# Performance work log

Measured on AMD Instinct MI355X. Metric: run time of the kernel, lower is better.

Reference implementation:

```python
import jax, jax.numpy as jnp
import numpy as np

DIM = 1024
NUM_HEADS = 16
HEAD_DIM = DIM // NUM_HEADS
B, T = 2, 2048


def _rope_tables(seq_len, head_dim, dtype=jnp.float32):
    inv_freq = 1.0 / (10000.0 ** (jnp.arange(0, head_dim, 2, dtype=jnp.float32) / head_dim))
    t = jnp.arange(seq_len, dtype=jnp.float32)
    freqs = jnp.einsum('i,j->ij', t, inv_freq)            # [T, head_dim/2]
    emb = jnp.concatenate((freqs, freqs), axis=-1)         # [T, head_dim]
    return jnp.cos(emb).astype(dtype), jnp.sin(emb).astype(dtype)


def _rotate_half(x):
    x1, x2 = x[..., : x.shape[-1] // 2], x[..., x.shape[-1] // 2 :]
    return jnp.concatenate((-x2, x1), axis=-1)


def setup_inputs() -> dict:
    key = jax.random.key(0)
    ks = jax.random.split(key, 5)
    s = 1.0 / np.sqrt(DIM)
    return {
        'x': jax.random.normal(ks[0], (B, T, DIM), dtype=jnp.float32),
        'w_q': jax.random.normal(ks[1], (DIM, DIM), dtype=jnp.float32) * s,
        'w_k': jax.random.normal(ks[2], (DIM, DIM), dtype=jnp.float32) * s,
        'w_v': jax.random.normal(ks[3], (DIM, DIM), dtype=jnp.float32) * s,
        'w_out': jax.random.normal(ks[4], (DIM, DIM), dtype=jnp.float32) * s,
    }


def reference(x, w_q, w_k, w_v, w_out):
    Bn, Tn, C = x.shape
    scale = HEAD_DIM ** -0.5
    # nn.Linear(bias=False): y = x @ W^T; reshape to [B, H, T, Dh]
    def proj(w):
        y = jnp.einsum('btc,dc->btd', x, w)
        return y.reshape(Bn, Tn, NUM_HEADS, HEAD_DIM).transpose(0, 2, 1, 3)
    q, k, v = proj(w_q), proj(w_k), proj(w_v)
    cos, sin = _rope_tables(Tn, HEAD_DIM, x.dtype)         # [T, Dh], broadcasts over B,H
    q = q * cos + _rotate_half(q) * sin
    k = k * cos + _rotate_half(k) * sin
    attn = jnp.einsum('bhqd,bhkd->bhqk', q, k) * scale     # [B,H,T,T]
    attn = jax.nn.softmax(attn, axis=-1)
    out = jnp.einsum('bhqk,bhkd->bhqd', attn, v)           # [B,H,T,Dh]
    out = out.transpose(0, 2, 1, 3).reshape(Bn, Tn, C)
    return jnp.einsum('btc,dc->btd', out, w_out)
```

## Files before the change

kernel.cpp:

```cpp
#include <hip/hip_runtime.h>


typedef _Float16 f16;
typedef f16 f16x8 __attribute__((ext_vector_type(8)));
typedef __fp16 fp16x2 __attribute__((ext_vector_type(2)));
typedef float f32x4 __attribute__((ext_vector_type(4)));
typedef float f32x16 __attribute__((ext_vector_type(16)));
typedef unsigned int u32;
typedef unsigned short u16;

union V16 { uint4 u; f16x8 h; };

__device__ __forceinline__ float exp2_fast(float x) {
#if __has_builtin(__builtin_amdgcn_exp2f)
  return __builtin_amdgcn_exp2f(x);
#else
  return __expf(x * 0.69314718056f);
#endif
}

__device__ __forceinline__ u32 pkrtz(float a, float b) {
  union { fp16x2 h; u32 u; } cv;
  cv.h = __builtin_amdgcn_cvt_pkrtz(a, b);
  return cv.u;
}

#define PLSWAP(a, b)                                                          \
  asm volatile("s_nop 1\n\tv_permlane32_swap_b32 %0, %1" : "+v"(a), "+v"(b))

#define GLDS(src, dst) __builtin_amdgcn_global_load_lds(                      \
    (const __attribute__((address_space(1))) void*)(const void*)(src),        \
    (__attribute__((address_space(3))) void*)(void*)(dst), 16, 0, 0)

__global__ __launch_bounds__(256) void rope_tables_kernel(float* __restrict__ cosT,
                                                          float* __restrict__ sinT) {
  int i = blockIdx.x * 256 + threadIdx.x;
  int t = i >> 5, j = i & 31;
  float inv = 1.0f / powf(10000.0f, (float)(2 * j) * (1.0f / 64.0f));
  float ang = (float)t * inv;
  double a = (double)ang;
  cosT[i] = (float)cos(a);
  sinT[i] = (float)sin(a);
}

__global__ __launch_bounds__(256)
void cvt5_kernel(const float* __restrict__ x,  const float* __restrict__ wq,
                 const float* __restrict__ wk, const float* __restrict__ wv,
                 const float* __restrict__ wo,
                 f16* __restrict__ xh, f16* __restrict__ W3,
                 f16* __restrict__ woh) {
  int bx = blockIdx.x;
  const float* src; f16* dst; int i;
  if (bx < 4096) {
    src = x; dst = xh; i = bx * 256 + threadIdx.x;
  } else {
    int b = (bx - 4096) >> 10;
    i = ((bx - 4096) & 1023) * 256 + threadIdx.x;
    src = (b == 0) ? wq : (b == 1) ? wk : (b == 2) ? wv : wo;
    dst = (b == 3) ? woh : W3 + (size_t)b * 1048576;
  }
  float4 v = ((const float4*)src)[i];
  union { f16 h[4]; uint2 u; } cv;
  cv.h[0] = (f16)v.x; cv.h[1] = (f16)v.y; cv.h[2] = (f16)v.z; cv.h[3] = (f16)v.w;
  ((uint2*)dst)[i] = cv.u;
}

__global__ __launch_bounds__(256)
void gemm_qkv_kernel(const f16* __restrict__ X,
                     const f16* __restrict__ W3,
                     f16* __restrict__ Qo, f16* __restrict__ Ko,
                     f16* __restrict__ VTo,
                     const float* __restrict__ cosT,
                     const float* __restrict__ sinT) {
  __shared__ u16 lds[2][8192];

  const int tid = threadIdx.x, lane = tid & 63, w = tid >> 6;
  const int c = lane & 15, g = lane >> 4;
  const int m0 = blockIdx.x * 128;
  const int by = blockIdx.y;
  const int wsel = by >> 3, hp = by & 7, h0 = hp * 2;
  const f16* Wb = W3 + (size_t)wsel * (1024 * 1024) + (size_t)hp * 128 * 1024;

  const int n1 = tid, n2 = tid + 256;
  const int r1 = n1 >> 2, gc1 = (n1 & 3) ^ ((n1 >> 3) & 3);
  const int r2 = n2 >> 2, gc2 = (n2 & 3) ^ ((n2 >> 3) & 3);
  const f16* gA1 = X + (size_t)(m0 + r1) * 1024 + gc1 * 8;
  const f16* gA2 = X + (size_t)(m0 + r2) * 1024 + gc2 * 8;
  const f16* gB1 = Wb + (size_t)r1 * 1024 + gc1 * 8;
  const f16* gB2 = Wb + (size_t)r2 * 1024 + gc2 * 8;
  const int dA1 = n1 * 8, dA2 = n2 * 8;
  const int dB1 = 4096 + n1 * 8, dB2 = 4096 + n2 * 8;

  f32x4 acc[2][8];
  const f32x4 zero = {0.f, 0.f, 0.f, 0.f};
#pragma unroll
  for (int mi = 0; mi < 2; ++mi)
#pragma unroll
    for (int ni = 0; ni < 8; ++ni) acc[mi][ni] = zero;

#define STAGE_QKV(buf, kt) do {                                               \
    const int ko = (kt) * 32;                                                 \
    GLDS(gA1 + ko, &lds[buf][dA1]);                                           \
    GLDS(gA2 + ko, &lds[buf][dA2]);                                           \
    GLDS(gB1 + ko, &lds[buf][dB1]);                                           \
    GLDS(gB2 + ko, &lds[buf][dB2]);                                           \
  } while (0)

  const int swz = (g ^ ((c >> 1) & 3)) * 8;

  STAGE_QKV(0, 0);
  __syncthreads();
  for (int kt = 0; kt < 32; ++kt) {
    const int cur = kt & 1;
    if (kt < 31) STAGE_QKV(cur ^ 1, kt + 1);
    V16 a[2], b[8];
#pragma unroll
    for (int mi = 0; mi < 2; ++mi)
      a[mi].u = *(const uint4*)&lds[cur][(w * 32 + mi * 16 + c) * 32 + swz];
#pragma unroll
    for (int ni = 0; ni < 8; ++ni)
      b[ni].u = *(const uint4*)&lds[cur][4096 + (ni * 16 + c) * 32 + swz];
    __builtin_amdgcn_s_setprio(1);
#pragma unroll
    for (int mi = 0; mi < 2; ++mi)
#pragma unroll
      for (int ni = 0; ni < 8; ++ni)
        acc[mi][ni] = __builtin_amdgcn_mfma_f32_16x16x32_f16(a[mi].h, b[ni].h, acc[mi][ni], 0, 0, 0);
    __builtin_amdgcn_s_setprio(0);
    __syncthreads();
  }

  if (wsel < 2) {
    f16* Out = (wsel == 0) ? Qo : Ko;
    const float psc = (wsel == 0) ? 0.18033688f : 1.0f;
#pragma unroll
    for (int mi = 0; mi < 2; ++mi)
#pragma unroll
      for (int r = 0; r < 4; ++r) {
        int m = m0 + w * 32 + mi * 16 + g * 4 + r;
        int bb = m >> 11, t = m & 2047;
        float co0 = cosT[t * 32 + c],      si0 = sinT[t * 32 + c];
        float co1 = cosT[t * 32 + 16 + c], si1 = sinT[t * 32 + 16 + c];
#pragma unroll
        for (int ni = 0; ni < 8; ++ni) {
          int head = h0 + (ni >> 2);
          int d = (ni & 3) * 16 + c;
          float co = (ni & 1) ? co1 : co0;
          float si = (ni & 1) ? si1 : si0;
          float partner = acc[mi][ni ^ 2][r];
          float v = (acc[mi][ni][r] * co + ((d < 32) ? -partner : partner) * si) * psc;
          Out[((size_t)(bb * 16 + head) * 2048 + t) * 64 + d] = (f16)v;
        }
      }
  } else {
    u16* sT = &lds[0][0];
    const int bbv = m0 >> 11;
    const int t0 = (m0 & 2047) + w * 32;
#pragma unroll
    for (int p = 0; p < 2; ++p) {
#pragma unroll
      for (int mi = 0; mi < 2; ++mi)
#pragma unroll
        for (int nn = 0; nn < 4; ++nn)
#pragma unroll
          for (int r = 0; r < 4; ++r) {
            int ni = p * 4 + nn;
            int dl = nn * 16 + c;
            int tl = mi * 16 + g * 4 + r;
            union { f16 h; u16 u; } cv; cv.h = (f16)acc[mi][ni][r];
            sT[w * 2560 + dl * 40 + tl] = cv.u;
          }
      f16* dst = VTo + ((size_t)(bbv * 16 + h0 + p) * 64 + lane) * 2048 + t0;
      const u16* srcp = &sT[w * 2560 + lane * 40];
      *(uint4*)(dst +  0) = *(const uint4*)(srcp +  0);
      *(uint4*)(dst +  8) = *(const uint4*)(srcp +  8);
      *(uint4*)(dst + 16) = *(const uint4*)(srcp + 16);
      *(uint4*)(dst + 24) = *(const uint4*)(srcp + 24);
    }
  }
}

__global__ __launch_bounds__(256)
void gemm_out_kernel(const f16* __restrict__ AH, const f16* __restrict__ BH,
                     float* __restrict__ outF) {
  __shared__ u16 lds[2][6144];

  const int tid = threadIdx.x, lane = tid & 63, w = tid >> 6;
  const int c = lane & 15, g = lane >> 4;
  const int m0 = blockIdx.x * 128, n0 = blockIdx.y * 64;

  const int n1 = tid, n2 = tid + 256;
  const int r1 = n1 >> 2, gc1 = (n1 & 3) ^ ((n1 >> 3) & 3);
  const int r2 = n2 >> 2, gc2 = (n2 & 3) ^ ((n2 >> 3) & 3);
  const f16* gA1 = AH + (size_t)(m0 + r1) * 1024 + gc1 * 8;
  const f16* gA2 = AH + (size_t)(m0 + r2) * 1024 + gc2 * 8;
  const f16* gB1 = BH + (size_t)(n0 + r1) * 1024 + gc1 * 8;
  const int dA1 = n1 * 8, dA2 = n2 * 8;
  const int dB1 = 4096 + n1 * 8;

  f32x4 acc[2][4];
  const f32x4 zero = {0.f, 0.f, 0.f, 0.f};
#pragma unroll
  for (int mi = 0; mi < 2; ++mi)
#pragma unroll
    for (int ni = 0; ni < 4; ++ni) acc[mi][ni] = zero;

#define STAGE_OUT(buf, kt) do {                                               \
    const int ko = (kt) * 32;                                                 \
    GLDS(gA1 + ko, &lds[buf][dA1]);                                           \
    GLDS(gA2 + ko, &lds[buf][dA2]);                                           \
    GLDS(gB1 + ko, &lds[buf][dB1]);                                           \
  } while (0)

  const int swz = (g ^ ((c >> 1) & 3)) * 8;

  STAGE_OUT(0, 0);
  __syncthreads();
  for (int kt = 0; kt < 32; ++kt) {
    const int cur = kt & 1;
    if (kt < 31) STAGE_OUT(cur ^ 1, kt + 1);
    V16 a[2], b[4];
#pragma unroll
    for (int mi = 0; mi < 2; ++mi)
      a[mi].u = *(const uint4*)&lds[cur][(w * 32 + mi * 16 + c) * 32 + swz];
#pragma unroll
    for (int ni = 0; ni < 4; ++ni)
      b[ni].u = *(const uint4*)&lds[cur][4096 + (ni * 16 + c) * 32 + swz];
    __builtin_amdgcn_s_setprio(1);
#pragma unroll
    for (int mi = 0; mi < 2; ++mi)
#pragma unroll
      for (int ni = 0; ni < 4; ++ni)
        acc[mi][ni] = __builtin_amdgcn_mfma_f32_16x16x32_f16(a[mi].h, b[ni].h, acc[mi][ni], 0, 0, 0);
    __builtin_amdgcn_s_setprio(0);
    __syncthreads();
  }

#pragma unroll
  for (int mi = 0; mi < 2; ++mi)
#pragma unroll
    for (int r = 0; r < 4; ++r) {
      int m = m0 + w * 32 + mi * 16 + g * 4 + r;
#pragma unroll
      for (int ni = 0; ni < 4; ++ni)
        outF[(size_t)m * 1024 + n0 + ni * 16 + c] = acc[mi][ni][r];
    }
}

__global__ __launch_bounds__(256)
void attn_kernel(const f16* __restrict__ Q, const f16* __restrict__ K,
                 const f16* __restrict__ VT, f16* __restrict__ OH) {
  __shared__ u16 sK[64 * 64];
  __shared__ u16 sV[64 * 64];
  __shared__ u16 sT16[4][32][36];

  const int tid = threadIdx.x, lane = tid & 63, wid = tid >> 6;
  const int q32 = lane & 31, hi = lane >> 5;
  const int hh = blockIdx.y, bb = blockIdx.z, bh = bb * 16 + hh;
  const int q0 = blockIdx.x * 128 + wid * 32;

  V16 qf[4];
  const f16* qp = Q + ((size_t)bh * 2048 + q0 + q32) * 64 + 8 * hi;
#pragma unroll
  for (int kd = 0; kd < 4; ++kd)
    qf[kd].u = *(const uint4*)(qp + 16 * kd);

  f32x16 o0 = 0.0f, o1 = 0.0f;
  float m_run = -1e30f, l_run = 0.f;

  const int srow = tid >> 3, scol = tid & 7;
  const f16* gK = K  + ((size_t)bh * 2048 + srow) * 64 + scol * 8;
  const f16* gV = VT + ((size_t)bh * 64 + srow) * 2048 + scol * 8;
  const int dst0 = srow * 128 + ((scol ^ (srow & 7)) << 4);
  const int dst1 = dst0 + 32 * 128;

  uint4 rk0, rk1, rv0, rv1;
#define LOADT(kt) do {                                                        \
    const f16* pk = gK + (size_t)(kt) * 4096;                                 \
    rk0 = *(const uint4*)(pk);                                                \
    rk1 = *(const uint4*)(pk + 32 * 64);                                      \
    const f16* pv = gV + (size_t)(kt) * 64;                                   \
    rv0 = *(const uint4*)(pv);                                                \
    rv1 = *(const uint4*)(pv + 32 * 2048);                                    \
  } while (0)
#define WRITET() do {                                                         \
    *(uint4*)((char*)sK + dst0) = rk0; *(uint4*)((char*)sK + dst1) = rk1;     \
    *(uint4*)((char*)sV + dst0) = rv0; *(uint4*)((char*)sV + dst1) = rv1;     \
  } while (0)

  const int swzrow = (q32 & 7) << 4;

  LOADT(0);
  WRITET();
  __syncthreads();

  for (int kt = 0; kt < 32; ++kt) {
    if (kt < 31) LOADT(kt + 1);

    f32x16 st0 = 0.0f, st1 = 0.0f;
    __builtin_amdgcn_s_setprio(1);
#pragma unroll
    for (int kd = 0; kd < 4; ++kd) {
      const int off = ((32 * kd + 16 * hi) ^ swzrow);
      V16 kf0, kf1;
      kf0.u = *(const uint4*)((const char*)sK + q32 * 128 + off);
      kf1.u = *(const uint4*)((const char*)sK + (32 + q32) * 128 + off);
      st0 = __builtin_amdgcn_mfma_f32_32x32x16_f16(kf0.h, qf[kd].h, st0, 0, 0, 0);
      st1 = __builtin_amdgcn_mfma_f32_32x32x16_f16(kf1.h, qf[kd].h, st1, 0, 0, 0);
    }
    __builtin_amdgcn_s_setprio(0);

    float mx = st0[0];
#pragma unroll
    for (int r = 1; r < 16; ++r) mx = fmaxf(mx, st0[r]);
#pragma unroll
    for (int r = 0; r < 16; ++r) mx = fmaxf(mx, st1[r]);
    mx = fmaxf(mx, __shfl_xor(mx, 32, 64));
    if (!__all(mx <= m_run + 11.5415603f)) {
      float mnew = fmaxf(m_run, mx);
      float alpha = exp2_fast(m_run - mnew);
      m_run = mnew;
      l_run *= alpha;
      o0 *= alpha;
      o1 *= alpha;
    }
    float sum = 0.f;
    u32 c0[8], c1[8];
#pragma unroll
    for (int m = 0; m < 8; ++m) {
      float p0 = exp2_fast(st0[2 * m] - m_run);
      float p1 = exp2_fast(st0[2 * m + 1] - m_run);
      sum += p0 + p1;
      c0[m] = pkrtz(p0, p1);
      float p2 = exp2_fast(st1[2 * m] - m_run);
      float p3 = exp2_fast(st1[2 * m + 1] - m_run);
      sum += p2 + p3;
      c1[m] = pkrtz(p2, p3);
    }
    sum += __shfl_xor(sum, 32, 64);
    l_run += sum;

    V16 pB[4];
    {
      u32 y0 = c0[0], x0 = c0[2]; PLSWAP(y0, x0);
      u32 y1 = c0[1], x1 = c0[3]; PLSWAP(y1, x1);
      pB[0].u.x = y0; pB[0].u.y = y1; pB[0].u.z = x0; pB[0].u.w = x1;
      u32 y2 = c0[4], x2 = c0[6]; PLSWAP(y2, x2);
      u32 y3 = c0[5], x3 = c0[7]; PLSWAP(y3, x3);
      pB[1].u.x = y2; pB[1].u.y = y3; pB[1].u.z = x2; pB[1].u.w = x3;
      u32 y4 = c1[0], x4 = c1[2]; PLSWAP(y4, x4);
      u32 y5 = c1[1], x5 = c1[3]; PLSWAP(y5, x5);
      pB[2].u.x = y4; pB[2].u.y = y5; pB[2].u.z = x4; pB[2].u.w = x5;
      u32 y6 = c1[4], x6 = c1[6]; PLSWAP(y6, x6);
      u32 y7 = c1[5], x7 = c1[7]; PLSWAP(y7, x7);
      pB[3].u.x = y6; pB[3].u.y = y7; pB[3].u.z = x6; pB[3].u.w = x7;
    }

    __builtin_amdgcn_s_setprio(1);
#pragma unroll
    for (int ks = 0; ks < 4; ++ks) {
      const int off = ((32 * ks + 16 * hi) ^ swzrow);
      V16 vf0, vf1;
      vf0.u = *(const uint4*)((const char*)sV + q32 * 128 + off);
      vf1.u = *(const uint4*)((const char*)sV + (32 + q32) * 128 + off);
      o0 = __builtin_amdgcn_mfma_f32_32x32x16_f16(vf0.h, pB[ks].h, o0, 0, 0, 0);
      o1 = __builtin_amdgcn_mfma_f32_32x32x16_f16(vf1.h, pB[ks].h, o1, 0, 0, 0);
    }
    __builtin_amdgcn_s_setprio(0);

    __syncthreads();
    if (kt < 31) WRITET();
    __syncthreads();
  }

  const float inv = 1.0f / l_run;
  const int qr = lane >> 1, dh = (lane & 1) * 16;
#pragma unroll
  for (int dt = 0; dt < 2; ++dt) {
#pragma unroll
    for (int r = 0; r < 16; ++r) {
      float v = (dt ? o1[r] : o0[r]) * inv;
      union { f16 h; u16 u; } cv; cv.h = (f16)v;
      sT16[wid][q32][(r & 3) + 8 * (r >> 2) + 4 * hi] = cv.u;
    }
    __syncthreads();
    const u16* sp = &sT16[wid][qr][dh];
    uint2 a0 = *(const uint2*)(sp + 0),  a1 = *(const uint2*)(sp + 4);
    uint2 a2 = *(const uint2*)(sp + 8),  a3 = *(const uint2*)(sp + 12);
    size_t gbase = ((size_t)bb * 2048 + q0 + qr) * 1024 + hh * 64 + 32 * dt + dh;
    *(uint2*)(OH + gbase + 0)  = a0;
    *(uint2*)(OH + gbase + 4)  = a1;
    *(uint2*)(OH + gbase + 8)  = a2;
    *(uint2*)(OH + gbase + 12) = a3;
    __syncthreads();
  }
}

extern "C" void kernel_launch(void* const* d_in, const int* in_sizes, int n_in,
                              void* d_out, int out_size, void* d_ws, size_t ws_size,
                              hipStream_t stream) {
  const float* x  = (const float*)d_in[0];
  const float* wq = (const float*)d_in[1];
  const float* wk = (const float*)d_in[2];
  const float* wv = (const float*)d_in[3];
  const float* wo = (const float*)d_in[4];

  constexpr size_t SZ_X   = 4096ull * 1024 * 2;
  constexpr size_t SZ_W   = 1024ull * 1024 * 2;
  constexpr size_t SZ_QKV = 2ull * 16 * 2048 * 64 * 2;
  constexpr size_t SZ_TBL = 2048ull * 32 * 4;
  constexpr size_t NEED = SZ_X + 4 * SZ_W + 3 * SZ_QKV + 2 * SZ_TBL;
  if (ws_size < NEED) return;

  char* ws = (char*)d_ws;
  f16* xh  = (f16*)(ws);
  f16* W3  = (f16*)(ws + SZ_X);
  f16* woh = (f16*)(ws + SZ_X + 3 * SZ_W);
  char* p  = ws + SZ_X + 4 * SZ_W;
  f16* qb  = (f16*)(p);            p += SZ_QKV;
  f16* kb  = (f16*)(p);            p += SZ_QKV;
  f16* vT  = (f16*)(p);            p += SZ_QKV;
  float* cosT = (float*)(p);       p += SZ_TBL;
  float* sinT = (float*)(p);
  f16* oh = xh;

  rope_tables_kernel<<<256, 256, 0, stream>>>(cosT, sinT);
  cvt5_kernel<<<8192, 256, 0, stream>>>(x, wq, wk, wv, wo, xh, W3, woh);

  gemm_qkv_kernel<<<dim3(32, 24), 256, 0, stream>>>(xh, W3, qb, kb, vT,
                                                    cosT, sinT);

  attn_kernel<<<dim3(16, 16, 2), 256, 0, stream>>>(qb, kb, vT, oh);

  gemm_out_kernel<<<dim3(32, 16), 256, 0, stream>>>(oh, woh, (float*)d_out);
}
```

Baseline: 137.8 us.

## Software-pipeline attention with triple-buffered K/V and overlapped QK^T/PV

```diff
diff --git a/kernel.cpp b/kernel.cpp
--- a/kernel.cpp
+++ b/kernel.cpp
@@ -247,17 +247,19 @@
     }
 }
 
-__global__ __launch_bounds__(256)
+__global__ __launch_bounds__(256, 2)
 void attn_kernel(const f16* __restrict__ Q, const f16* __restrict__ K,
                  const f16* __restrict__ VT, f16* __restrict__ OH) {
-  __shared__ u16 sK[64 * 64];
-  __shared__ u16 sV[64 * 64];
+  __shared__ u16 sKV[3][8192];
   __shared__ u16 sT16[4][32][36];
 
   const int tid = threadIdx.x, lane = tid & 63, wid = tid >> 6;
   const int q32 = lane & 31, hi = lane >> 5;
-  const int hh = blockIdx.y, bb = blockIdx.z, bh = bb * 16 + hh;
-  const int q0 = blockIdx.x * 128 + wid * 32;
+  const int bx = blockIdx.x;
+  const int bh = (bx & 7) + 8 * (bx >> 7);
+  const int qt = (bx >> 3) & 15;
+  const int bb = bh >> 4, hh = bh & 15;
+  const int q0 = qt * 128 + wid * 32;
 
   V16 qf[4];
   const f16* qp = Q + ((size_t)bh * 2048 + q0 + q32) * 64 + 8 * hi;
@@ -283,95 +285,105 @@
     rv0 = *(const uint4*)(pv);                                                \
     rv1 = *(const uint4*)(pv + 32 * 2048);                                    \
   } while (0)
-#define WRITET() do {                                                         \
-    *(uint4*)((char*)sK + dst0) = rk0; *(uint4*)((char*)sK + dst1) = rk1;     \
-    *(uint4*)((char*)sV + dst0) = rv0; *(uint4*)((char*)sV + dst1) = rv1;     \
+#define WRITET(buf) do {                                                      \
+    char* base_ = (char*)&sKV[buf][0];                                        \
+    *(uint4*)(base_ + dst0) = rk0; *(uint4*)(base_ + dst1) = rk1;             \
+    *(uint4*)(base_ + 8192 + dst0) = rv0; *(uint4*)(base_ + 8192 + dst1) = rv1;\
   } while (0)
 
   const int swzrow = (q32 & 7) << 4;
 
+#define QKT(D0, D1, buf) do {                                                 \
+    const char* kb_ = (const char*)&sKV[buf][0];                              \
+    __builtin_amdgcn_s_setprio(1);                                            \
+    _Pragma("unroll")                                                         \
+    for (int kd = 0; kd < 4; ++kd) {                                          \
+      const int off = ((32 * kd + 16 * hi) ^ swzrow);                         \
+      V16 kf0, kf1;                                                           \
+      kf0.u = *(const uint4*)(kb_ + q32 * 128 + off);                         \
+      kf1.u = *(const uint4*)(kb_ + (32 + q32) * 128 + off);                  \
+      D0 = __builtin_amdgcn_mfma_f32_32x32x16_f16(kf0.h, qf[kd].h, D0, 0, 0, 0);\
+      D1 = __builtin_amdgcn_mfma_f32_32x32x16_f16(kf1.h, qf[kd].h, D1, 0, 0, 0);\
+    }                                                                         \
+    __builtin_amdgcn_s_setprio(0);                                            \
+  } while (0)
+
+#define SOFTMAX_PB() do {                                                     \
+    float mx = st0[0];                                                        \
+    _Pragma("unroll")                                                         \
+    for (int r = 1; r < 16; ++r) mx = fmaxf(mx, st0[r]);                      \
+    _Pragma("unroll")                                                         \
+    for (int r = 0; r < 16; ++r) mx = fmaxf(mx, st1[r]);                      \
+    mx = fmaxf(mx, __shfl_xor(mx, 32, 64));                                   \
+    if (!__all(mx <= m_run + 11.5415603f)) {                                  \
+      float mnew = fmaxf(m_run, mx);                                          \
+      float alpha = exp2_fast(m_run - mnew);                                  \
+      m_run = mnew; l_run *= alpha; o0 *= alpha; o1 *= alpha;                 \
+    }                                                                         \
+    float sum = 0.f;                                                          \
+    u32 c0[8], c1[8];                                                         \
+    _Pragma("unroll")                                                         \
+    for (int m = 0; m < 8; ++m) {                                             \
+      float p0 = exp2_fast(st0[2 * m] - m_run);                               \
+      float p1 = exp2_fast(st0[2 * m + 1] - m_run);                           \
+      sum += p0 + p1; c0[m] = pkrtz(p0, p1);                                  \
+      float p2 = exp2_fast(st1[2 * m] - m_run);                               \
+      float p3 = exp2_fast(st1[2 * m + 1] - m_run);                           \
+      sum += p2 + p3; c1[m] = pkrtz(p2, p3);                                  \
+    }                                                                         \
+    sum += __shfl_xor(sum, 32, 64);                                           \
+    l_run += sum;                                                             \
+    { u32 y0 = c0[0], x0 = c0[2]; PLSWAP(y0, x0);                             \
+      u32 y1 = c0[1], x1 = c0[3]; PLSWAP(y1, x1);                             \
+      pB[0].u.x = y0; pB[0].u.y = y1; pB[0].u.z = x0; pB[0].u.w = x1;         \
+      u32 y2 = c0[4], x2 = c0[6]; PLSWAP(y2, x2);                             \
+      u32 y3 = c0[5], x3 = c0[7]; PLSWAP(y3, x3);                             \
+      pB[1].u.x = y2; pB[1].u.y = y3; pB[1].u.z = x2; pB[1].u.w = x3;         \
+      u32 y4 = c1[0], x4 = c1[2]; PLSWAP(y4, x4);                             \
+      u32 y5 = c1[1], x5 = c1[3]; PLSWAP(y5, x5);                             \
+      pB[2].u.x = y4; pB[2].u.y = y5; pB[2].u.z = x4; pB[2].u.w = x5;         \
+      u32 y6 = c1[4], x6 = c1[6]; PLSWAP(y6, x6);                             \
+      u32 y7 = c1[5], x7 = c1[7]; PLSWAP(y7, x7);                             \
+      pB[3].u.x = y6; pB[3].u.y = y7; pB[3].u.z = x6; pB[3].u.w = x7; }       \
+  } while (0)
+
+#define PVOP(buf) do {                                                        \
+    const char* vb_ = (const char*)&sKV[buf][0] + 8192;                       \
+    __builtin_amdgcn_s_setprio(1);                                            \
+    _Pragma("unroll")                                                         \
+    for (int ks = 0; ks < 4; ++ks) {                                          \
+      const int off = ((32 * ks + 16 * hi) ^ swzrow);                         \
+      V16 vf0, vf1;                                                           \
+      vf0.u = *(const uint4*)(vb_ + q32 * 128 + off);                         \
+      vf1.u = *(const uint4*)(vb_ + (32 + q32) * 128 + off);                  \
+      o0 = __builtin_amdgcn_mfma_f32_32x32x16_f16(vf0.h, pB[ks].h, o0, 0, 0, 0);\
+      o1 = __builtin_amdgcn_mfma_f32_32x32x16_f16(vf1.h, pB[ks].h, o1, 0, 0, 0);\
+    }                                                                         \
+    __builtin_amdgcn_s_setprio(0);                                            \
+  } while (0)
+
   LOADT(0);
-  WRITET();
+  WRITET(0);
   __syncthreads();
-
-  for (int kt = 0; kt < 32; ++kt) {
-    if (kt < 31) LOADT(kt + 1);
-
-    f32x16 st0 = 0.0f, st1 = 0.0f;
-    __builtin_amdgcn_s_setprio(1);
-#pragma unroll
-    for (int kd = 0; kd < 4; ++kd) {
-      const int off = ((32 * kd + 16 * hi) ^ swzrow);
-      V16 kf0, kf1;
-      kf0.u = *(const uint4*)((const char*)sK + q32 * 128 + off);
-      kf1.u = *(const uint4*)((const char*)sK + (32 + q32) * 128 + off);
-      st0 = __builtin_amdgcn_mfma_f32_32x32x16_f16(kf0.h, qf[kd].h, st0, 0, 0, 0);
-      st1 = __builtin_amdgcn_mfma_f32_32x32x16_f16(kf1.h, qf[kd].h, st1, 0, 0, 0);
-    }
-    __builtin_amdgcn_s_setprio(0);
-
-    float mx = st0[0];
-#pragma unroll
-    for (int r = 1; r < 16; ++r) mx = fmaxf(mx, st0[r]);
-#pragma unroll
-    for (int r = 0; r < 16; ++r) mx = fmaxf(mx, st1[r]);
-    mx = fmaxf(mx, __shfl_xor(mx, 32, 64));
-    if (!__all(mx <= m_run + 11.5415603f)) {
-      float mnew = fmaxf(m_run, mx);
-      float alpha = exp2_fast(m_run - mnew);
-      m_run = mnew;
-      l_run *= alpha;
-      o0 *= alpha;
-      o1 *= alpha;
-    }
-    float sum = 0.f;
-    u32 c0[8], c1[8];
-#pragma unroll
-    for (int m = 0; m < 8; ++m) {
-      float p0 = exp2_fast(st0[2 * m] - m_run);
-      float p1 = exp2_fast(st0[2 * m + 1] - m_run);
-      sum += p0 + p1;
-      c0[m] = pkrtz(p0, p1);
-      float p2 = exp2_fast(st1[2 * m] - m_run);
-      float p3 = exp2_fast(st1[2 * m + 1] - m_run);
-      sum += p2 + p3;
-      c1[m] = pkrtz(p2, p3);
-    }
-    sum += __shfl_xor(sum, 32, 64);
-    l_run += sum;
-
-    V16 pB[4];
-    {
-      u32 y0 = c0[0], x0 = c0[2]; PLSWAP(y0, x0);
-      u32 y1 = c0[1], x1 = c0[3]; PLSWAP(y1, x1);
-      pB[0].u.x = y0; pB[0].u.y = y1; pB[0].u.z = x0; pB[0].u.w = x1;
-      u32 y2 = c0[4], x2 = c0[6]; PLSWAP(y2, x2);
-      u32 y3 = c0[5], x3 = c0[7]; PLSWAP(y3, x3);
-      pB[1].u.x = y2; pB[1].u.y = y3; pB[1].u.z = x2; pB[1].u.w = x3;
-      u32 y4 = c1[0], x4 = c1[2]; PLSWAP(y4, x4);
-      u32 y5 = c1[1], x5 = c1[3]; PLSWAP(y5, x5);
-      pB[2].u.x = y4; pB[2].u.y = y5; pB[2].u.z = x4; pB[2].u.w = x5;
-      u32 y6 = c1[4], x6 = c1[6]; PLSWAP(y6, x6);
-      u32 y7 = c1[5], x7 = c1[7]; PLSWAP(y7, x7);
-      pB[3].u.x = y6; pB[3].u.y = y7; pB[3].u.z = x6; pB[3].u.w = x7;
-    }
-
-    __builtin_amdgcn_s_setprio(1);
-#pragma unroll
-    for (int ks = 0; ks < 4; ++ks) {
-      const int off = ((32 * ks + 16 * hi) ^ swzrow);
-      V16 vf0, vf1;
-      vf0.u = *(const uint4*)((const char*)sV + q32 * 128 + off);
-      vf1.u = *(const uint4*)((const char*)sV + (32 + q32) * 128 + off);
-      o0 = __builtin_amdgcn_mfma_f32_32x32x16_f16(vf0.h, pB[ks].h, o0, 0, 0, 0);
-      o1 = __builtin_amdgcn_mfma_f32_32x32x16_f16(vf1.h, pB[ks].h, o1, 0, 0, 0);
-    }
-    __builtin_amdgcn_s_setprio(0);
-
+  LOADT(1);
+  f32x16 st0 = 0.0f, st1 = 0.0f;
+  QKT(st0, st1, 0);
+
+  V16 pB[4];
+  int bw = 1, bp = 0;
+  for (int kt = 0; kt < 31; ++kt) {
+    WRITET(bw);
     __syncthreads();
-    if (kt < 31) WRITET();
-    __syncthreads();
-  }
+    if (kt < 30) LOADT(kt + 2);
+    f32x16 sn0 = 0.0f, sn1 = 0.0f;
+    QKT(sn0, sn1, bw);
+    SOFTMAX_PB();
+    PVOP(bp);
+    st0 = sn0; st1 = sn1;
+    bp = bw; bw = (bw == 2) ? 0 : bw + 1;
+  }
+  SOFTMAX_PB();
+  PVOP(bp);
 
   const float inv = 1.0f / l_run;
   const int qr = lane >> 1, dh = (lane & 1) * 16;
@@ -430,7 +442,7 @@
   gemm_qkv_kernel<<<dim3(32, 24), 256, 0, stream>>>(xh, W3, qb, kb, vT,
                                                     cosT, sinT);
 
-  attn_kernel<<<dim3(16, 16, 2), 256, 0, stream>>>(qb, kb, vT, oh);
+  attn_kernel<<<512, 256, 0, stream>>>(qb, kb, vT, oh);
 
   gemm_out_kernel<<<dim3(32, 16), 256, 0, stream>>>(oh, woh, (float*)d_out);
 }
```

After: 136.9 us. Within noise of the previous version (-0.6%).
